# Kernel optimization log

Measured on AMD Instinct MI355X. Metric: run time of the kernel, lower is better.

Reference implementation:

```python
import jax, jax.numpy as jnp
import numpy as np

BN_EPS = 1e-5


def setup_inputs() -> dict:
    key = jax.random.key(0)
    ks = jax.random.split(key, 7)
    B, C, N = 8, 512, 2048
    P = C // 2
    x = jax.random.normal(ks[0], (B, C, N), dtype=jnp.float32)
    # 1x1 conv weights (no bias), shape [out, in]
    Wg = jax.random.normal(ks[1], (P, C), dtype=jnp.float32) * (1.0 / np.sqrt(C))
    Wtheta = jax.random.normal(ks[2], (P, C), dtype=jnp.float32) * (1.0 / np.sqrt(C))
    Wphi = jax.random.normal(ks[3], (P, C), dtype=jnp.float32) * (1.0 / np.sqrt(C))
    Wz = jax.random.normal(ks[4], (C, P), dtype=jnp.float32) * (1.0 / np.sqrt(P))
    gamma = jnp.ones((C,), dtype=jnp.float32)
    beta = jnp.zeros((C,), dtype=jnp.float32)
    return {"x": x, "Wg": Wg, "Wtheta": Wtheta, "Wphi": Wphi, "Wz": Wz,
            "gamma": gamma, "beta": beta}


def reference(x, Wg, Wtheta, Wphi, Wz, gamma, beta):
    # x: [B, C, N]
    g = jnp.einsum('pc,bcn->bnp', Wg, x)        # [B, N, P]
    theta = jnp.einsum('pc,bcn->bnp', Wtheta, x)  # [B, N, P]
    phi = jnp.einsum('pc,bcn->bpn', Wphi, x)      # [B, P, N]
    f = jnp.einsum('bnp,bpm->bnm', theta, phi)    # [B, N, N] unscaled scores
    f = jax.nn.softmax(f, axis=-1)
    y = jnp.einsum('bnm,bmp->bpn', f, g)          # [B, P, N]
    z = jnp.einsum('cp,bpn->bcn', Wz, y)          # [B, C, N]
    # BatchNorm1d (training-mode batch stats over batch and length dims)
    mean = jnp.mean(z, axis=(0, 2), keepdims=True)
    var = jnp.mean((z - mean) ** 2, axis=(0, 2), keepdims=True)
    z_bn = (z - mean) / jnp.sqrt(var + BN_EPS)
    z_bn = z_bn * gamma[None, :, None] + beta[None, :, None]
    return z_bn + x
```

## Files before the change

### kernel.cpp

```cpp
#include <hip/hip_runtime.h>
#include <hip/hip_bf16.h>


typedef __attribute__((ext_vector_type(8))) short short8;
typedef __attribute__((ext_vector_type(4))) float floatx4;

__device__ __forceinline__ unsigned short f2bf(float v) {
    __hip_bfloat16 h = __float2bfloat16(v);
    return *(unsigned short*)&h;
}
__device__ __forceinline__ float bf2f(unsigned short u) {
    __hip_bfloat16 h;
    *(unsigned short*)&h = u;
    return __bfloat162float(h);
}

__global__ __launch_bounds__(256) void transpose_split(
    const float* __restrict__ X, unsigned short* __restrict__ Thi,
    unsigned short* __restrict__ Tlo, int R, int N)
{
    X   += (long)blockIdx.z * R * N;
    Thi += (long)blockIdx.z * N * R;
    Tlo += (long)blockIdx.z * N * R;
    __shared__ float s[32][33];
    const int tx = threadIdx.x & 31, ty = threadIdx.x >> 5;
    const int n0 = blockIdx.x * 32, r0 = blockIdx.y * 32;
#pragma unroll
    for (int r = 0; r < 4; ++r)
        s[ty + r * 8][tx] = X[(long)(r0 + ty + r * 8) * N + n0 + tx];
    __syncthreads();
#pragma unroll
    for (int r = 0; r < 4; ++r) {
        const int n = ty + r * 8;
        const float v = s[tx][n];
        const unsigned short hi = f2bf(v);
        const unsigned short lo = f2bf(v - bf2f(hi));
        Thi[(long)(n0 + n) * R + r0 + tx] = hi;
        Tlo[(long)(n0 + n) * R + r0 + tx] = lo;
    }
}

__global__ __launch_bounds__(256) void split_w2(
    const float* __restrict__ Wth, const float* __restrict__ Wph,
    unsigned short* __restrict__ Whi, unsigned short* __restrict__ Wlo, int PC)
{
    const int i = blockIdx.x * 256 + threadIdx.x;
    if (i < 2 * PC) {
        const float v = (i < PC) ? Wth[i] : Wph[i - PC];
        const unsigned short hi = f2bf(v);
        Whi[i] = hi;
        Wlo[i] = f2bf(v - bf2f(hi));
    }
}

__global__ __launch_bounds__(256) void cast_bf16(
    const float* __restrict__ X, unsigned short* __restrict__ Y)
{
    const long i = ((long)blockIdx.x * 256 + threadIdx.x) * 4;
    const float4 v = *(const float4*)&X[i];
    ushort4 o;
    o.x = f2bf(v.x); o.y = f2bf(v.y); o.z = f2bf(v.z); o.w = f2bf(v.w);
    *(ushort4*)&Y[i] = o;
}

#define BK 32

template <bool SPLIT, int OUTMODE, int FM, int FN>
__global__ __launch_bounds__(256) void mfma_gemm(
    const unsigned short* __restrict__ Ahi, const unsigned short* __restrict__ Alo,
    const unsigned short* __restrict__ Bhi, const unsigned short* __restrict__ Blo,
    void* __restrict__ Cout, void* __restrict__ Cout2,
    int K, int lda, int ldb, int ldc,
    long sA, long sB, long sC,
    float* __restrict__ S1, float* __restrict__ S2)
{
    constexpr int MTM = FM * 32, MTN = FN * 32;
    constexpr int SA = FM / 2, SB = FN / 2;

    Ahi += (long)blockIdx.z * sA;
    Bhi += (long)blockIdx.z * sB;
    if (SPLIT) { Alo += (long)blockIdx.z * sA; Blo += (long)blockIdx.z * sB; }
    float* Cf = (float*)Cout + (long)blockIdx.z * sC;
    unsigned short* Ch = (unsigned short*)Cout + (long)blockIdx.z * sC;
    unsigned short* Cl = (unsigned short*)Cout2 + (long)blockIdx.z * sC;

    __shared__ unsigned short AsH[MTM * BK], BsH[MTN * BK];
    __shared__ unsigned short AsL[SPLIT ? MTM * BK : 8], BsL[SPLIT ? MTN * BK : 8];

    const int tid = threadIdx.x;
    const int wid = tid >> 6, lane = tid & 63;
    const int wm = (wid >> 1) * (FM * 16), wn = (wid & 1) * (FN * 16);
    const int l15 = lane & 15, quad = lane >> 4;
    const int m0 = blockIdx.y * MTM, n0 = blockIdx.x * MTN;

    int arow[SA], acol[SA], brow[SB], bcol[SB];
#pragma unroll
    for (int t = 0; t < SA; ++t) {
        const int gid = t * 256 + tid;
        arow[t] = gid >> 2; acol[t] = (gid & 3) * 8;
    }
#pragma unroll
    for (int t = 0; t < SB; ++t) {
        const int gid = t * 256 + tid;
        brow[t] = gid >> 2; bcol[t] = (gid & 3) * 8;
    }

    short8 pa[SA], pb[SB], paL[SPLIT ? SA : 1], pbL[SPLIT ? SB : 1];

    auto loadTiles = [&](int k0) {
#pragma unroll
        for (int t = 0; t < SA; ++t) {
            const long o = (long)(m0 + arow[t]) * lda + k0 + acol[t];
            pa[t] = *(const short8*)&Ahi[o];
            if (SPLIT) paL[t] = *(const short8*)&Alo[o];
        }
#pragma unroll
        for (int t = 0; t < SB; ++t) {
            const long o = (long)(n0 + brow[t]) * ldb + k0 + bcol[t];
            pb[t] = *(const short8*)&Bhi[o];
            if (SPLIT) pbL[t] = *(const short8*)&Blo[o];
        }
    };
    auto writeTiles = [&]() {
#pragma unroll
        for (int t = 0; t < SA; ++t) {
            *(short8*)&AsH[arow[t] * BK + acol[t]] = pa[t];
            if (SPLIT) *(short8*)&AsL[arow[t] * BK + acol[t]] = paL[t];
        }
#pragma unroll
        for (int t = 0; t < SB; ++t) {
            *(short8*)&BsH[brow[t] * BK + bcol[t]] = pb[t];
            if (SPLIT) *(short8*)&BsL[brow[t] * BK + bcol[t]] = pbL[t];
        }
    };

    floatx4 acc[FM][FN];
#pragma unroll
    for (int i = 0; i < FM; ++i)
#pragma unroll
        for (int j = 0; j < FN; ++j) acc[i][j] = (floatx4){0.f, 0.f, 0.f, 0.f};

    const int iters = K / BK;
    loadTiles(0);
    writeTiles();
    __syncthreads();

    for (int it = 0; it < iters; ++it) {
        if (it + 1 < iters) loadTiles((it + 1) * BK);

        short8 ah[FM], bh[FN], al[SPLIT ? FM : 1], bl[SPLIT ? FN : 1];
#pragma unroll
        for (int i = 0; i < FM; ++i) {
            ah[i] = *(const short8*)&AsH[(wm + i * 16 + l15) * BK + quad * 8];
            if (SPLIT) al[i] = *(const short8*)&AsL[(wm + i * 16 + l15) * BK + quad * 8];
        }
#pragma unroll
        for (int j = 0; j < FN; ++j) {
            bh[j] = *(const short8*)&BsH[(wn + j * 16 + l15) * BK + quad * 8];
            if (SPLIT) bl[j] = *(const short8*)&BsL[(wn + j * 16 + l15) * BK + quad * 8];
        }
#pragma unroll
        for (int i = 0; i < FM; ++i)
#pragma unroll
            for (int j = 0; j < FN; ++j) {
                acc[i][j] = __builtin_amdgcn_mfma_f32_16x16x32_bf16(ah[i], bh[j], acc[i][j], 0, 0, 0);
                if (SPLIT) {
                    acc[i][j] = __builtin_amdgcn_mfma_f32_16x16x32_bf16(ah[i], bl[j], acc[i][j], 0, 0, 0);
                    acc[i][j] = __builtin_amdgcn_mfma_f32_16x16x32_bf16(al[i], bh[j], acc[i][j], 0, 0, 0);
                }
            }

        if (it + 1 < iters) {
            __syncthreads();
            writeTiles();
            __syncthreads();
        }
    }

#pragma unroll
    for (int i = 0; i < FM; ++i)
#pragma unroll
        for (int j = 0; j < FN; ++j) {
            const int m = m0 + wm + i * 16 + quad * 4;
            const int n = n0 + wn + j * 16 + l15;
#pragma unroll
            for (int r = 0; r < 4; ++r) {
                const float v = acc[i][j][r];
                const long idx = (long)(m + r) * ldc + n;
                if (OUTMODE == 0) {
                    Cf[idx] = v;
                } else if (OUTMODE == 1 || OUTMODE == 3) {
                    Ch[idx] = f2bf(v);
                } else {
                    const unsigned short hi = f2bf(v);
                    Ch[idx] = hi;
                    Cl[idx] = f2bf(v - bf2f(hi));
                }
            }
        }

    if (OUTMODE == 3) {
        const int slot = (blockIdx.z * gridDim.x + blockIdx.x) * 2 + (wn >> 6);
#pragma unroll
        for (int i = 0; i < FM; ++i)
#pragma unroll
            for (int r = 0; r < 4; ++r) {
                float s = 0.f, q = 0.f;
#pragma unroll
                for (int j = 0; j < FN; ++j) {
                    const float v = acc[i][j][r];
                    s += v; q += v * v;
                }
#pragma unroll
                for (int msk = 1; msk < 16; msk <<= 1) {
                    s += __shfl_xor(s, msk, 64);
                    q += __shfl_xor(q, msk, 64);
                }
                if (l15 == 0) {
                    const int row = m0 + wm + i * 16 + quad * 4 + r;
                    S1[(long)row * 256 + slot] = s;
                    S2[(long)row * 256 + slot] = q;
                }
            }
    }
}

#define FSTR 72
#define GSTR 72
#define PSTRP 136

__global__ __launch_bounds__(256, 2) void fused_attn(
    const unsigned short* __restrict__ thphH,
    const unsigned short* __restrict__ thphL,
    const unsigned short* __restrict__ gbf,
    float* __restrict__ yp,
    float2* __restrict__ ml)
{
    const int N = 2048, P = 256, P2 = 512;
    const int id = blockIdx.x;
    const int b  = id & 7;
    const int kh = (id >> 3) & 1;
    const int qt = id >> 4;
    const int q0 = qt * 64;

    const unsigned short* thB = thphH + (long)b * N * P2;
    const unsigned short* tlB = thphL + (long)b * N * P2;
    const unsigned short* gB  = gbf   + (long)b * P * N;
    float*  ypB = yp + (long)kh * (8L * N * P) + (long)b * N * P;
    float2* mlB = ml + (long)kh * (8L * N) + (long)b * N;

    __shared__ unsigned short FG[2 * 128 * FSTR];
    unsigned short* Fh = FG;
    unsigned short* Fl = FG + 128 * FSTR;
    unsigned short* Gs = FG;
    __shared__ unsigned short Pw[4][16 * PSTRP];

    const int tid = threadIdx.x;
    const int wid = tid >> 6, lane = tid & 63;
    const int l15 = lane & 15, quad = lane >> 4;

    short8 tHr[8], tLr[8];
    {
        const unsigned short* t1 = thB + (long)(q0 + wid * 16 + l15) * P2;
        const unsigned short* t2 = tlB + (long)(q0 + wid * 16 + l15) * P2;
#pragma unroll
        for (int kt = 0; kt < 8; ++kt) {
            tHr[kt] = *(const short8*)&t1[kt * 32 + quad * 8];
            tLr[kt] = *(const short8*)&t2[kt * 32 + quad * 8];
        }
    }

    float mrun[4], lrun[4];
#pragma unroll
    for (int r = 0; r < 4; ++r) { mrun[r] = -1e30f; lrun[r] = 0.f; }

    floatx4 oacc[16];
#pragma unroll
    for (int p = 0; p < 16; ++p) oacc[p] = (floatx4){0.f, 0.f, 0.f, 0.f};

    const int prow = tid >> 3, pc8 = (tid & 7) * 8;
    short8 pfH[4], pfL[4], pg[8];

    auto loadPhi = [&](int m0, int kc) {
#pragma unroll
        for (int s = 0; s < 4; ++s) {
            const long o = (long)(m0 + prow + s * 32) * P2 + P + kc * 64 + pc8;
            pfH[s] = *(const short8*)&thB[o];
            pfL[s] = *(const short8*)&tlB[o];
        }
    };
    auto writePhi = [&]() {
#pragma unroll
        for (int s = 0; s < 4; ++s) {
            *(short8*)&Fh[(prow + s * 32) * FSTR + pc8] = pfH[s];
            *(short8*)&Fl[(prow + s * 32) * FSTR + pc8] = pfL[s];
        }
    };
    auto loadG = [&](int m0, int mc) {
#pragma unroll
        for (int s = 0; s < 8; ++s)
            pg[s] = *(const short8*)&gB[(long)(prow + s * 32) * N + m0 + mc * 64 + pc8];
    };
    auto writeG = [&]() {
#pragma unroll
        for (int s = 0; s < 8; ++s)
            *(short8*)&Gs[(prow + s * 32) * GSTR + pc8] = pg[s];
    };

    for (int mt = 0; mt < 8; ++mt) {
        const int m0 = kh * 1024 + mt * 128;

        floatx4 sacc[8];
#pragma unroll
        for (int j = 0; j < 8; ++j) sacc[j] = (floatx4){0.f, 0.f, 0.f, 0.f};

        loadPhi(m0, 0);
        __syncthreads();
        writePhi();
        __syncthreads();
#pragma unroll
        for (int kc = 0; kc < 4; ++kc) {
            if (kc < 3) loadPhi(m0, kc + 1);
#pragma unroll
            for (int ks = 0; ks < 2; ++ks) {
                const short8 aH = tHr[kc * 2 + ks];
                const short8 aL = tLr[kc * 2 + ks];
#pragma unroll
                for (int j = 0; j < 8; ++j) {
                    const int ro = (j * 16 + l15) * FSTR + ks * 32 + quad * 8;
                    const short8 bh = *(const short8*)&Fh[ro];
                    const short8 bl = *(const short8*)&Fl[ro];
                    sacc[j] = __builtin_amdgcn_mfma_f32_16x16x32_bf16(aH, bh, sacc[j], 0, 0, 0);
                    sacc[j] = __builtin_amdgcn_mfma_f32_16x16x32_bf16(aH, bl, sacc[j], 0, 0, 0);
                    sacc[j] = __builtin_amdgcn_mfma_f32_16x16x32_bf16(aL, bh, sacc[j], 0, 0, 0);
                }
            }
            if (kc < 3) {
                __syncthreads();
                writePhi();
                __syncthreads();
            }
        }

        float alpha[4];
#pragma unroll
        for (int r = 0; r < 4; ++r) {
            float v = sacc[0][r];
#pragma unroll
            for (int j = 1; j < 8; ++j) v = fmaxf(v, sacc[j][r]);
            v = fmaxf(v, __shfl_xor(v, 1, 64));
            v = fmaxf(v, __shfl_xor(v, 2, 64));
            v = fmaxf(v, __shfl_xor(v, 4, 64));
            v = fmaxf(v, __shfl_xor(v, 8, 64));
            const float mo = mrun[r];
            const float mn = fmaxf(mo, v);
            mrun[r] = mn;
            alpha[r] = __expf(mo - mn);
        }
        float lpart[4] = {0.f, 0.f, 0.f, 0.f};
#pragma unroll
        for (int j = 0; j < 8; ++j)
#pragma unroll
            for (int r = 0; r < 4; ++r) {
                const float p = __expf(sacc[j][r] - mrun[r]);
                Pw[wid][(quad * 4 + r) * PSTRP + j * 16 + l15] = f2bf(p);
                lpart[r] += p;
            }
#pragma unroll
        for (int r = 0; r < 4; ++r) {
            float s = lpart[r];
            s += __shfl_xor(s, 1, 64);
            s += __shfl_xor(s, 2, 64);
            s += __shfl_xor(s, 4, 64);
            s += __shfl_xor(s, 8, 64);
            lrun[r] = lrun[r] * alpha[r] + s;
        }
        {
            const int noresc = (alpha[0] == 1.f) & (alpha[1] == 1.f) &
                               (alpha[2] == 1.f) & (alpha[3] == 1.f);
            if (!__all(noresc)) {
#pragma unroll
                for (int p = 0; p < 16; ++p)
#pragma unroll
                    for (int r = 0; r < 4; ++r) oacc[p][r] *= alpha[r];
            }
        }

        loadG(m0, 0);
        __syncthreads();
        writeG();
        __syncthreads();
#pragma unroll
        for (int mc = 0; mc < 2; ++mc) {
            if (mc == 0) loadG(m0, 1);
#pragma unroll
            for (int kk = 0; kk < 2; ++kk) {
                const short8 af = *(const short8*)&Pw[wid][l15 * PSTRP + mc * 64 + kk * 32 + quad * 8];
#pragma unroll
                for (int pj = 0; pj < 16; ++pj) {
                    const short8 bg = *(const short8*)&Gs[(pj * 16 + l15) * GSTR + kk * 32 + quad * 8];
                    oacc[pj] = __builtin_amdgcn_mfma_f32_16x16x32_bf16(af, bg, oacc[pj], 0, 0, 0);
                }
            }
            if (mc == 0) {
                __syncthreads();
                writeG();
                __syncthreads();
            }
        }
    }

    float linv[4];
#pragma unroll
    for (int r = 0; r < 4; ++r) linv[r] = 1.0f / lrun[r];
#pragma unroll
    for (int pj = 0; pj < 16; ++pj)
#pragma unroll
        for (int r = 0; r < 4; ++r) {
            const int row = q0 + wid * 16 + quad * 4 + r;
            const int col = pj * 16 + l15;
            ypB[(long)row * P + col] = oacc[pj][r] * linv[r];
        }
    if (l15 == 0) {
#pragma unroll
        for (int r = 0; r < 4; ++r) {
            const int row = q0 + wid * 16 + quad * 4 + r;
            mlB[row] = float2{mrun[r], lrun[r]};
        }
    }
}

__global__ __launch_bounds__(256) void attn_merge(
    const float* __restrict__ yp, const float2* __restrict__ ml,
    unsigned short* __restrict__ ybf)
{
    const long HALF = 8L * 2048 * 256;
    const long t = (long)blockIdx.x * 256 + threadIdx.x;
    const long row = t >> 5;
    const int  c0  = ((int)t & 31) * 8;
    const float2 a = ml[row];
    const float2 c = ml[8L * 2048 + row];
    const float mx = fmaxf(a.x, c.x);
    const float w1 = a.y * __expf(a.x - mx);
    const float w2 = c.y * __expf(c.x - mx);
    const float inv = 1.0f / (w1 + w2);
    const float f1 = w1 * inv, f2 = w2 * inv;
    const long base = row * 256 + c0;
    const float4 u0 = *(const float4*)&yp[base];
    const float4 u1 = *(const float4*)&yp[base + 4];
    const float4 v0 = *(const float4*)&yp[HALF + base];
    const float4 v1 = *(const float4*)&yp[HALF + base + 4];
    ushort4 o0, o1;
    o0.x = f2bf(f1 * u0.x + f2 * v0.x);
    o0.y = f2bf(f1 * u0.y + f2 * v0.y);
    o0.z = f2bf(f1 * u0.z + f2 * v0.z);
    o0.w = f2bf(f1 * u0.w + f2 * v0.w);
    o1.x = f2bf(f1 * u1.x + f2 * v1.x);
    o1.y = f2bf(f1 * u1.y + f2 * v1.y);
    o1.z = f2bf(f1 * u1.z + f2 * v1.z);
    o1.w = f2bf(f1 * u1.w + f2 * v1.w);
    *(ushort4*)&ybf[base] = o0;
    *(ushort4*)&ybf[base + 4] = o1;
}

__global__ __launch_bounds__(256) void bn_finalize(
    const float* __restrict__ p1, const float* __restrict__ p2,
    float* __restrict__ mean, float* __restrict__ rstd, float cnt)
{
    const int c = blockIdx.x, t = threadIdx.x;
    __shared__ float rs[256], rq[256];
    rs[t] = p1[(long)c * 256 + t];
    rq[t] = p2[(long)c * 256 + t];
    __syncthreads();
    for (int st = 128; st > 0; st >>= 1) {
        if (t < st) { rs[t] += rs[t + st]; rq[t] += rq[t + st]; }
        __syncthreads();
    }
    if (t == 0) {
        const float m = rs[0] / cnt;
        mean[c] = m;
        rstd[c] = rsqrtf(rq[0] / cnt - m * m + 1e-5f);
    }
}

__global__ __launch_bounds__(256) void bn_apply_bf(
    const unsigned short* __restrict__ z, const float* __restrict__ x,
    const float* __restrict__ mean, const float* __restrict__ rstd,
    const float* __restrict__ gamma, const float* __restrict__ beta,
    float* __restrict__ out, int C, int N)
{
    const long i = ((long)blockIdx.x * 256 + threadIdx.x) * 8;
    const int c = (int)((i / N) % C);
    const float mu = mean[c], rs = rstd[c], ga = gamma[c], be = beta[c];
    const ushort4 z0 = *(const ushort4*)&z[i];
    const ushort4 z1 = *(const ushort4*)&z[i + 4];
    const float4 x0 = *(const float4*)&x[i];
    const float4 x1 = *(const float4*)&x[i + 4];
    float4 o0, o1;
    o0.x = (bf2f(z0.x) - mu) * rs * ga + be + x0.x;
    o0.y = (bf2f(z0.y) - mu) * rs * ga + be + x0.y;
    o0.z = (bf2f(z0.z) - mu) * rs * ga + be + x0.z;
    o0.w = (bf2f(z0.w) - mu) * rs * ga + be + x0.w;
    o1.x = (bf2f(z1.x) - mu) * rs * ga + be + x1.x;
    o1.y = (bf2f(z1.y) - mu) * rs * ga + be + x1.y;
    o1.z = (bf2f(z1.z) - mu) * rs * ga + be + x1.z;
    o1.w = (bf2f(z1.w) - mu) * rs * ga + be + x1.w;
    *(float4*)&out[i] = o0;
    *(float4*)&out[i + 4] = o1;
}

extern "C" void kernel_launch(void* const* d_in, const int* in_sizes, int n_in,
                              void* d_out, int out_size, void* d_ws, size_t ws_size,
                              hipStream_t stream)
{
    const int B = 8, C = 512, N = 2048, P = 256;
    const float* x      = (const float*)d_in[0];
    const float* Wg     = (const float*)d_in[1];
    const float* Wtheta = (const float*)d_in[2];
    const float* Wphi   = (const float*)d_in[3];
    const float* Wz     = (const float*)d_in[4];
    const float* gamma  = (const float*)d_in[5];
    const float* beta   = (const float*)d_in[6];
    float* out = (float*)d_out;

    float* ws = (float*)d_ws;
    const long NCle = (long)N * C;
    const long NP   = (long)N * P;
    const long R0   = (long)B * NCle;
    unsigned short* xtH   = (unsigned short*)ws;
    unsigned short* xtL   = xtH + B * NCle;
    unsigned short* zbf   = (unsigned short*)ws;
    unsigned short* thphH = (unsigned short*)(ws + R0);
    unsigned short* thphL = thphH + B * NCle;
    unsigned short* gbf   = (unsigned short*)(ws + 2 * R0);
    unsigned short* fbf   = gbf + B * NP;
    unsigned short* ybf   = fbf + (long)B * N * N;
    unsigned short* W2H   = ybf + B * NP;
    unsigned short* W2L   = W2H + 2L * P * C;
    unsigned short* WgB   = W2L + 2L * P * C;
    unsigned short* WzB   = WgB + (long)P * C;
    float*          yp    = (float*)fbf;
    float2*         ml    = (float2*)(yp + 2L * B * NP);
    float*          bnp1  = ws + R0;
    float*          bnp2  = bnp1 + (long)C * 256;
    float*          mean  = bnp2 + (long)C * 256;
    float*          rstd  = mean + C;

    const long sX = (long)C * N;
    const int  P2 = 2 * P;

    transpose_split<<<dim3(N / 32, C / 32, B), 256, 0, stream>>>(x, xtH, xtL, C, N);
    split_w2<<<(2 * P * C + 255) / 256, 256, 0, stream>>>(Wtheta, Wphi, W2H, W2L, P * C);
    cast_bf16<<<P * C / 1024, 256, 0, stream>>>(Wg, WgB);
    cast_bf16<<<P * C / 1024, 256, 0, stream>>>(Wz, WzB);

    mfma_gemm<true, 2, 4, 4><<<dim3(P2 / 128, N / 128, B), 256, 0, stream>>>(
        xtH, xtL, W2H, W2L, thphH, thphL, C, C, C, P2, NCle, 0, NCle, nullptr, nullptr);
    mfma_gemm<false, 1, 2, 4><<<dim3(N / 128, P / 64, B), 256, 0, stream>>>(
        WgB, WgB, xtH, xtH, gbf, gbf, C, C, C, N, 0, NCle, NP, nullptr, nullptr);

    fused_attn<<<dim3(512), 256, 0, stream>>>(thphH, thphL, gbf, yp, ml);
    attn_merge<<<dim3((int)((2L * B * NP / 8) / 256 / 2)), 256, 0, stream>>>(yp, ml, ybf);

    mfma_gemm<false, 3, 4, 4><<<dim3(N / 128, C / 128, B), 256, 0, stream>>>(
        WzB, WzB, ybf, ybf, zbf, zbf, P, P, P, N, 0, NP, sX, bnp1, bnp2);

    bn_finalize<<<C, 256, 0, stream>>>(bnp1, bnp2, mean, rstd, (float)B * N);
    bn_apply_bf<<<(int)((B * sX) / 2048), 256, 0, stream>>>(zbf, x, mean, rstd, gamma, beta, out, C, N);
}
```

Before: 273.7 us.

## Split attention key range four ways and halve shared-memory staging chunks

The fused attention kernel now splits the key dimension into four partitions instead of two, doubling the grid to 1024 blocks, and the merge kernel combines four partial results with their max/sum statistics. Shared-memory staging chunks for phi and g shrink from 64 to 32 columns, reducing LDS and register use so the launch bound can request four blocks per SM. The goal is more parallelism and occupancy for the attention stage. The cost is more partial output traffic (four fp32 partials instead of two) written and read by the merge, and twice as many syncthreads pairs per tile. The ml buffer is relocated to a fixed workspace offset, presumably to make room for the larger partial buffer.

```diff
diff --git a/kernel.cpp b/kernel.cpp
--- a/kernel.cpp
+++ b/kernel.cpp
@@ -225,11 +225,11 @@
     }
 }
 
-#define FSTR 72
-#define GSTR 72
+#define FSTR 40
+#define GSTR 40
 #define PSTRP 136
 
-__global__ __launch_bounds__(256, 2) void fused_attn(
+__global__ __launch_bounds__(256, 4) void fused_attn(
     const unsigned short* __restrict__ thphH,
     const unsigned short* __restrict__ thphL,
     const unsigned short* __restrict__ gbf,
@@ -239,8 +239,8 @@
     const int N = 2048, P = 256, P2 = 512;
     const int id = blockIdx.x;
     const int b  = id & 7;
-    const int kh = (id >> 3) & 1;
-    const int qt = id >> 4;
+    const int kh = (id >> 3) & 3;
+    const int qt = id >> 5;
     const int q0 = qt * 64;
 
     const unsigned short* thB = thphH + (long)b * N * P2;
@@ -278,37 +278,37 @@
 #pragma unroll
     for (int p = 0; p < 16; ++p) oacc[p] = (floatx4){0.f, 0.f, 0.f, 0.f};
 
-    const int prow = tid >> 3, pc8 = (tid & 7) * 8;
-    short8 pfH[4], pfL[4], pg[8];
+    const int prow = tid >> 2, pc8 = (tid & 3) * 8;
+    short8 pfH[2], pfL[2], pg[4];
 
     auto loadPhi = [&](int m0, int kc) {
 #pragma unroll
-        for (int s = 0; s < 4; ++s) {
-            const long o = (long)(m0 + prow + s * 32) * P2 + P + kc * 64 + pc8;
+        for (int s = 0; s < 2; ++s) {
+            const long o = (long)(m0 + prow + s * 64) * P2 + P + kc * 32 + pc8;
             pfH[s] = *(const short8*)&thB[o];
             pfL[s] = *(const short8*)&tlB[o];
         }
     };
     auto writePhi = [&]() {
 #pragma unroll
-        for (int s = 0; s < 4; ++s) {
-            *(short8*)&Fh[(prow + s * 32) * FSTR + pc8] = pfH[s];
-            *(short8*)&Fl[(prow + s * 32) * FSTR + pc8] = pfL[s];
+        for (int s = 0; s < 2; ++s) {
+            *(short8*)&Fh[(prow + s * 64) * FSTR + pc8] = pfH[s];
+            *(short8*)&Fl[(prow + s * 64) * FSTR + pc8] = pfL[s];
         }
     };
     auto loadG = [&](int m0, int mc) {
 #pragma unroll
-        for (int s = 0; s < 8; ++s)
-            pg[s] = *(const short8*)&gB[(long)(prow + s * 32) * N + m0 + mc * 64 + pc8];
+        for (int s = 0; s < 4; ++s)
+            pg[s] = *(const short8*)&gB[(long)(prow + s * 64) * N + m0 + mc * 32 + pc8];
     };
     auto writeG = [&]() {
 #pragma unroll
-        for (int s = 0; s < 8; ++s)
-            *(short8*)&Gs[(prow + s * 32) * GSTR + pc8] = pg[s];
+        for (int s = 0; s < 4; ++s)
+            *(short8*)&Gs[(prow + s * 64) * GSTR + pc8] = pg[s];
     };
 
-    for (int mt = 0; mt < 8; ++mt) {
-        const int m0 = kh * 1024 + mt * 128;
+    for (int mt = 0; mt < 4; ++mt) {
+        const int m0 = kh * 512 + mt * 128;
 
         floatx4 sacc[8];
 #pragma unroll
@@ -319,23 +319,20 @@
         writePhi();
         __syncthreads();
 #pragma unroll
-        for (int kc = 0; kc < 4; ++kc) {
-            if (kc < 3) loadPhi(m0, kc + 1);
-#pragma unroll
-            for (int ks = 0; ks < 2; ++ks) {
-                const short8 aH = tHr[kc * 2 + ks];
-                const short8 aL = tLr[kc * 2 + ks];
-#pragma unroll
-                for (int j = 0; j < 8; ++j) {
-                    const int ro = (j * 16 + l15) * FSTR + ks * 32 + quad * 8;
-                    const short8 bh = *(const short8*)&Fh[ro];
-                    const short8 bl = *(const short8*)&Fl[ro];
-                    sacc[j] = __builtin_amdgcn_mfma_f32_16x16x32_bf16(aH, bh, sacc[j], 0, 0, 0);
-                    sacc[j] = __builtin_amdgcn_mfma_f32_16x16x32_bf16(aH, bl, sacc[j], 0, 0, 0);
-                    sacc[j] = __builtin_amdgcn_mfma_f32_16x16x32_bf16(aL, bh, sacc[j], 0, 0, 0);
-                }
-            }
-            if (kc < 3) {
+        for (int kc = 0; kc < 8; ++kc) {
+            if (kc < 7) loadPhi(m0, kc + 1);
+            const short8 aH = tHr[kc];
+            const short8 aL = tLr[kc];
+#pragma unroll
+            for (int j = 0; j < 8; ++j) {
+                const int ro = (j * 16 + l15) * FSTR + quad * 8;
+                const short8 bh = *(const short8*)&Fh[ro];
+                const short8 bl = *(const short8*)&Fl[ro];
+                sacc[j] = __builtin_amdgcn_mfma_f32_16x16x32_bf16(aH, bh, sacc[j], 0, 0, 0);
+                sacc[j] = __builtin_amdgcn_mfma_f32_16x16x32_bf16(aH, bl, sacc[j], 0, 0, 0);
+                sacc[j] = __builtin_amdgcn_mfma_f32_16x16x32_bf16(aL, bh, sacc[j], 0, 0, 0);
+            }
+            if (kc < 7) {
                 __syncthreads();
                 writePhi();
                 __syncthreads();
@@ -391,18 +388,15 @@
         writeG();
         __syncthreads();
 #pragma unroll
-        for (int mc = 0; mc < 2; ++mc) {
-            if (mc == 0) loadG(m0, 1);
-#pragma unroll
-            for (int kk = 0; kk < 2; ++kk) {
-                const short8 af = *(const short8*)&Pw[wid][l15 * PSTRP + mc * 64 + kk * 32 + quad * 8];
-#pragma unroll
-                for (int pj = 0; pj < 16; ++pj) {
-                    const short8 bg = *(const short8*)&Gs[(pj * 16 + l15) * GSTR + kk * 32 + quad * 8];
-                    oacc[pj] = __builtin_amdgcn_mfma_f32_16x16x32_bf16(af, bg, oacc[pj], 0, 0, 0);
-                }
-            }
-            if (mc == 0) {
+        for (int mc = 0; mc < 4; ++mc) {
+            if (mc < 3) loadG(m0, mc + 1);
+            const short8 af = *(const short8*)&Pw[wid][l15 * PSTRP + mc * 32 + quad * 8];
+#pragma unroll
+            for (int pj = 0; pj < 16; ++pj) {
+                const short8 bg = *(const short8*)&Gs[(pj * 16 + l15) * GSTR + quad * 8];
+                oacc[pj] = __builtin_amdgcn_mfma_f32_16x16x32_bf16(af, bg, oacc[pj], 0, 0, 0);
+            }
+            if (mc < 3) {
                 __syncthreads();
                 writeG();
                 __syncthreads();
@@ -434,31 +428,40 @@
     const float* __restrict__ yp, const float2* __restrict__ ml,
     unsigned short* __restrict__ ybf)
 {
-    const long HALF = 8L * 2048 * 256;
+    const long STRIDE = 8L * 2048 * 256;
+    const long NROWS  = 8L * 2048;
     const long t = (long)blockIdx.x * 256 + threadIdx.x;
     const long row = t >> 5;
     const int  c0  = ((int)t & 31) * 8;
-    const float2 a = ml[row];
-    const float2 c = ml[8L * 2048 + row];
-    const float mx = fmaxf(a.x, c.x);
-    const float w1 = a.y * __expf(a.x - mx);
-    const float w2 = c.y * __expf(c.x - mx);
-    const float inv = 1.0f / (w1 + w2);
-    const float f1 = w1 * inv, f2 = w2 * inv;
+    const float2 a0 = ml[row];
+    const float2 a1 = ml[NROWS + row];
+    const float2 a2 = ml[2 * NROWS + row];
+    const float2 a3 = ml[3 * NROWS + row];
+    const float mx = fmaxf(fmaxf(a0.x, a1.x), fmaxf(a2.x, a3.x));
+    const float w0 = a0.y * __expf(a0.x - mx);
+    const float w1 = a1.y * __expf(a1.x - mx);
+    const float w2 = a2.y * __expf(a2.x - mx);
+    const float w3 = a3.y * __expf(a3.x - mx);
+    const float inv = 1.0f / (w0 + w1 + w2 + w3);
+    const float f0 = w0 * inv, f1 = w1 * inv, f2 = w2 * inv, f3 = w3 * inv;
     const long base = row * 256 + c0;
     const float4 u0 = *(const float4*)&yp[base];
     const float4 u1 = *(const float4*)&yp[base + 4];
-    const float4 v0 = *(const float4*)&yp[HALF + base];
-    const float4 v1 = *(const float4*)&yp[HALF + base + 4];
+    const float4 v0 = *(const float4*)&yp[STRIDE + base];
+    const float4 v1 = *(const float4*)&yp[STRIDE + base + 4];
+    const float4 p0 = *(const float4*)&yp[2 * STRIDE + base];
+    const float4 p1 = *(const float4*)&yp[2 * STRIDE + base + 4];
+    const float4 q0 = *(const float4*)&yp[3 * STRIDE + base];
+    const float4 q1 = *(const float4*)&yp[3 * STRIDE + base + 4];
     ushort4 o0, o1;
-    o0.x = f2bf(f1 * u0.x + f2 * v0.x);
-    o0.y = f2bf(f1 * u0.y + f2 * v0.y);
-    o0.z = f2bf(f1 * u0.z + f2 * v0.z);
-    o0.w = f2bf(f1 * u0.w + f2 * v0.w);
-    o1.x = f2bf(f1 * u1.x + f2 * v1.x);
-    o1.y = f2bf(f1 * u1.y + f2 * v1.y);
-    o1.z = f2bf(f1 * u1.z + f2 * v1.z);
-    o1.w = f2bf(f1 * u1.w + f2 * v1.w);
+    o0.x = f2bf(f0 * u0.x + f1 * v0.x + f2 * p0.x + f3 * q0.x);
+    o0.y = f2bf(f0 * u0.y + f1 * v0.y + f2 * p0.y + f3 * q0.y);
+    o0.z = f2bf(f0 * u0.z + f1 * v0.z + f2 * p0.z + f3 * q0.z);
+    o0.w = f2bf(f0 * u0.w + f1 * v0.w + f2 * p0.w + f3 * q0.w);
+    o1.x = f2bf(f0 * u1.x + f1 * v1.x + f2 * p1.x + f3 * q1.x);
+    o1.y = f2bf(f0 * u1.y + f1 * v1.y + f2 * p1.y + f3 * q1.y);
+    o1.z = f2bf(f0 * u1.z + f1 * v1.z + f2 * p1.z + f3 * q1.z);
+    o1.w = f2bf(f0 * u1.w + f1 * v1.w + f2 * p1.w + f3 * q1.w);
     *(ushort4*)&ybf[base] = o0;
     *(ushort4*)&ybf[base + 4] = o1;
 }
@@ -540,7 +543,7 @@
     unsigned short* WgB   = W2L + 2L * P * C;
     unsigned short* WzB   = WgB + (long)P * C;
     float*          yp    = (float*)fbf;
-    float2*         ml    = (float2*)(yp + 2L * B * NP);
+    float2*         ml    = (float2*)(ws + 6L * 1024 * 1024);
     float*          bnp1  = ws + R0;
     float*          bnp2  = bnp1 + (long)C * 256;
     float*          mean  = bnp2 + (long)C * 256;
@@ -559,8 +562,8 @@
     mfma_gemm<false, 1, 2, 4><<<dim3(N / 128, P / 64, B), 256, 0, stream>>>(
         WgB, WgB, xtH, xtH, gbf, gbf, C, C, C, N, 0, NCle, NP, nullptr, nullptr);
 
-    fused_attn<<<dim3(512), 256, 0, stream>>>(thphH, thphL, gbf, yp, ml);
-    attn_merge<<<dim3((int)((2L * B * NP / 8) / 256 / 2)), 256, 0, stream>>>(yp, ml, ybf);
+    fused_attn<<<dim3(1024), 256, 0, stream>>>(thphH, thphL, gbf, yp, ml);
+    attn_merge<<<dim3(2048), 256, 0, stream>>>(yp, ml, ybf);
 
     mfma_gemm<false, 3, 4, 4><<<dim3(N / 128, C / 128, B), 256, 0, stream>>>(
         WzB, WzB, ybf, ybf, zbf, zbf, P, P, P, N, 0, NP, sX, bnp1, bnp2);
```

After: 411.5 us. 50.4% more time.
